# Kernel tuning notes

Measured on AMD Instinct MI355X. Metric: run time of the kernel, lower is better.

## Reference

```python
import jax, jax.numpy as jnp
import numpy as np

D_K = 128
NEG_BIG = 1e32  # matches torch's -1e+32 additive mask (finite in fp32)


def setup_inputs() -> dict:
    key = jax.random.key(0)
    kq, kk, kv, kqp, kkp = jax.random.split(key, 5)
    B, M, N, d_k, d_v = 8, 2048, 2048, D_K, 128
    return {
        "queries": jax.random.normal(kq, (B, M, d_k), dtype=jnp.float32),
        "keys": jax.random.normal(kk, (B, N, d_k), dtype=jnp.float32),
        "values": jax.random.normal(kv, (B, N, d_v), dtype=jnp.float32),
        "q_pres": jax.random.randint(kqp, (B, M), 0, 2, dtype=jnp.int32),
        "k_pres": jax.random.randint(kkp, (B, N), 0, 2, dtype=jnp.int32),
    }


def reference(queries, keys, values, q_pres, k_pres):
    # routing: [B, M, N] = Q K^T with multiplicative presence masking
    routing = jnp.einsum("bmd,bnd->bmn", queries, keys)
    qp = q_pres.astype(jnp.float32)  # [B, M]
    kp = k_pres.astype(jnp.float32)  # [B, N]
    routing = routing * qp[:, :, None]
    routing = routing * kp[:, None, :]
    # additive -1e32 mask for absent keys, then scaled softmax over N
    routing = routing - (1.0 - kp[:, None, :]) * NEG_BIG
    routing = jax.nn.softmax(routing / np.sqrt(D_K).astype(np.float32), axis=-1)
    return jnp.einsum("bmn,bnv->bmv", routing, values)
```

## Files before the change

### kernel.cpp

```cpp
#include <hip/hip_runtime.h>
#include <cstddef>
#include <cstdint>

#define SEQ_M 2048
#define SEQ_N 2048
#define DKV 128
#define BN 64
#define NCH 4
#define CHKEYS (SEQ_N / NCH)
#define NKT 32
#define MT2 16
#define NREC (NCH * 8 * MT2)

typedef _Float16 f16x8 __attribute__((ext_vector_type(8)));
typedef _Float16 f16x4 __attribute__((ext_vector_type(4)));
typedef _Float16 f16x2 __attribute__((ext_vector_type(2)));
typedef float f32x4 __attribute__((ext_vector_type(4)));
typedef float f32x16 __attribute__((ext_vector_type(16)));
typedef unsigned int u32x2 __attribute__((ext_vector_type(2)));
typedef unsigned int u32x4 __attribute__((ext_vector_type(4)));

#if defined(__has_builtin)
#if __has_builtin(__builtin_amdgcn_exp2f)
#define EXP2F(x) __builtin_amdgcn_exp2f(x)
#else
#define EXP2F(x) exp2f(x)
#endif
#else
#define EXP2F(x) exp2f(x)
#endif

#if defined(__has_builtin)
#if __has_builtin(__builtin_amdgcn_permlane32_swap)
#define HAVE_PLSWAP 1
#endif
#endif

#define SM_SCALE 0.12751745f
#define BIG_NEG 1.2751745e31f
#define MSHIFT 8.0f

#define KH_OFF 0
#define VH_OFF (256 * 8192)
#define P16_OFF (2 * 256 * 8192)
#define L_BYTE_OFF ((size_t)(P16_OFF + (size_t)NREC * 16384) * 2)
#define WS_NEED (L_BYTE_OFF + (size_t)NREC * 128 * 4)

#define AS1 __attribute__((address_space(1)))
#define AS3 __attribute__((address_space(3)))

__device__ __forceinline__ void copy16(const void* g, void* lds_base,
                                       void* lds_lane) {
#if defined(__has_builtin) && __has_builtin(__builtin_amdgcn_global_load_lds)
  __builtin_amdgcn_global_load_lds((const AS1 void*)g, (AS3 void*)lds_base, 16,
                                   0, 0);
  (void)lds_lane;
#else
  *(f16x8*)lds_lane = *(const f16x8*)g;
#endif
}

__device__ __forceinline__ void pswap(unsigned int a, unsigned int b, int hi,
                                      unsigned int& o0, unsigned int& o1) {
#if defined(HAVE_PLSWAP)
  u32x2 r = __builtin_amdgcn_permlane32_swap(a, b, false, false);
  o0 = r[0];
  o1 = r[1];
  (void)hi;
#else
  const unsigned int as = __shfl_xor(a, 32);
  const unsigned int bs = __shfl_xor(b, 32);
  o0 = hi ? bs : a;
  o1 = hi ? b : as;
#endif
}

__global__ __launch_bounds__(256) void prep(const float* __restrict__ Kg,
                                            const float* __restrict__ Vg,
                                            _Float16* __restrict__ Kh,
                                            _Float16* __restrict__ Vh) {
  const int T = blockIdx.x >> 2;
  const int kind = blockIdx.x & 1;
  const int half = (blockIdx.x >> 1) & 1;
  const int b = T >> 5, nt = T & 31;
  const int t = threadIdx.x;
  if (kind == 0) {
    const float* Kb = Kg + ((size_t)b * SEQ_N + nt * 64) * DKV;
    _Float16* Kt_ = Kh + (size_t)T * 8192;
#pragma unroll
    for (int i = 0; i < 2; ++i) {
      const int idx = half * 512 + i * 256 + t;
      const int c = idx & 15, key = idx >> 4;
      const float* src = Kb + key * DKV + c * 8;
      const float4 a0 = *(const float4*)src;
      const float4 a1 = *(const float4*)(src + 4);
      f16x8 h;
      h[0] = (_Float16)a0.x; h[1] = (_Float16)a0.y;
      h[2] = (_Float16)a0.z; h[3] = (_Float16)a0.w;
      h[4] = (_Float16)a1.x; h[5] = (_Float16)a1.y;
      h[6] = (_Float16)a1.z; h[7] = (_Float16)a1.w;
      *(f16x8*)&Kt_[c * 512 + key * 8] = h;
    }
  } else {
    const float* Vb = Vg + ((size_t)b * SEQ_N + nt * 64) * DKV;
    _Float16* Vt_ = Vh + (size_t)T * 8192;
#pragma unroll
    for (int i = 0; i < 2; ++i) {
      const int idx = half * 512 + i * 256 + t;
      const int vcol = idx & 127, g = idx >> 7;
      f16x8 h;
#pragma unroll
      for (int j = 0; j < 8; ++j)
        h[j] = (_Float16)Vb[(size_t)(g * 8 + j) * DKV + vcol];
      *(f16x8*)&Vt_[vcol * 64 + ((g ^ (vcol & 7)) * 8)] = h;
    }
  }
}

__global__ __launch_bounds__(256, 2) void attn_core7(
    const _Float16* __restrict__ Kh, const _Float16* __restrict__ Vh,
    const float* __restrict__ Qg, const int* __restrict__ QPg,
    const int* __restrict__ KPg, _Float16* __restrict__ P16,
    float* __restrict__ Lw) {
  __shared__ _Float16 smem[4 * 8192];
  _Float16* const Kt0 = smem;
  _Float16* const Vt0 = smem + 8192;
  _Float16* const Kt1 = smem + 16384;
  _Float16* const Vt1 = smem + 24576;

  const int tid = threadIdx.x;
  const int w = tid >> 6;
  const int lane = tid & 63;
  const int lam = lane & 31;
  const int hi = lane >> 5;

  const int b = blockIdx.x & 7;
  const int rest = blockIdx.x >> 3;
  const int mt = rest & 15;
  const int chk = rest >> 4;

  auto STAGE = [&](int nt, _Float16* ktD, _Float16* vtD) {
    const char* gsrc =
        (w < 2) ? (const char*)(Kh + (size_t)(b * NKT + nt) * 8192) + w * 8192
                : (const char*)(Vh + (size_t)(b * NKT + nt) * 8192) +
                      (w - 2) * 8192;
    char* ldst = (w < 2) ? (char*)ktD + w * 8192 : (char*)vtD + (w - 2) * 8192;
#pragma unroll
    for (int r = 0; r < 8; ++r)
      copy16(gsrc + r * 1024 + lane * 16, ldst + r * 1024,
             ldst + r * 1024 + lane * 16);
  };

  STAGE(chk * 8 + 0, Kt0, Vt0);

  const int qrow = mt * 128 + w * 32 + lam;
  const float* qptr = Qg + ((size_t)b * SEQ_M + qrow) * DKV;
  const float qs = QPg[b * SEQ_M + qrow] ? 1.0f : 0.0f;
  f16x8 qf[8];
#pragma unroll
  for (int ks16 = 0; ks16 < 8; ++ks16) {
    const float* src = qptr + ks16 * 16 + hi * 8;
    const float4 a0 = *(const float4*)src;
    const float4 a1 = *(const float4*)(src + 4);
    f16x8 h;
    h[0] = (_Float16)(a0.x * qs); h[1] = (_Float16)(a0.y * qs);
    h[2] = (_Float16)(a0.z * qs); h[3] = (_Float16)(a0.w * qs);
    h[4] = (_Float16)(a1.x * qs); h[5] = (_Float16)(a1.y * qs);
    h[6] = (_Float16)(a1.z * qs); h[7] = (_Float16)(a1.w * qs);
    qf[ks16] = h;
  }

  unsigned long long km[8];
#pragma unroll
  for (int ti = 0; ti < 8; ++ti)
    km[ti] = __ballot(
        KPg[(size_t)b * SEQ_N + (size_t)(chk * 8 + ti) * 64 + lane] != 0);

  f32x16 o[4];
#pragma unroll
  for (int vt = 0; vt < 4; ++vt)
#pragma unroll
    for (int r = 0; r < 16; ++r) o[vt][r] = 0.f;
  float pl = 0.f;

  __syncthreads();

#pragma unroll
  for (int ti = 0; ti < 8; ++ti) {
    _Float16* const KtC = (ti & 1) ? Kt1 : Kt0;
    _Float16* const VtC = (ti & 1) ? Vt1 : Vt0;
    _Float16* const KtN = (ti & 1) ? Kt0 : Kt1;
    _Float16* const VtN = (ti & 1) ? Vt0 : Vt1;
    if (ti + 1 < 8) STAGE(chk * 8 + ti + 1, KtN, VtN);
    const unsigned long long kmask = km[ti];

    f32x16 st0, st1;
#pragma unroll
    for (int r = 0; r < 16; ++r) { st0[r] = 0.f; st1[r] = 0.f; }
#pragma unroll
    for (int ks16 = 0; ks16 < 8; ++ks16) {
      const f16x8 qv = qf[ks16];
      const int c = ks16 * 2 + hi;
      const f16x8 k0 = *(const f16x8*)&KtC[c * 512 + (0 * 32 + lam) * 8];
      const f16x8 k1 = *(const f16x8*)&KtC[c * 512 + (1 * 32 + lam) * 8];
      st0 = __builtin_amdgcn_mfma_f32_32x32x16_f16(k0, qv, st0, 0, 0, 0);
      st1 = __builtin_amdgcn_mfma_f32_32x32x16_f16(k1, qv, st1, 0, 0, 0);
    }

    float p[2][16];
#pragma unroll
    for (int kt = 0; kt < 2; ++kt)
#pragma unroll
      for (int reg = 0; reg < 16; ++reg) {
        const int keybase = kt * 32 + (reg & 3) + 8 * (reg >> 2);
        const bool b0 = (kmask >> keybase) & 1ull;
        const bool b4 = (kmask >> (keybase + 4)) & 1ull;
        const float s = (kt ? st1[reg] : st0[reg]) * SM_SCALE - MSHIFT;
        const float e = EXP2F(s);
        const float v = (hi ? b4 : b0) ? e : 0.f;
        p[kt][reg] = v;
        pl += v;
      }

    unsigned int pk[2][8];
#pragma unroll
    for (int kt = 0; kt < 2; ++kt)
#pragma unroll
      for (int m = 0; m < 8; ++m) {
        f16x2 hh;
        hh[0] = (_Float16)p[kt][2 * m];
        hh[1] = (_Float16)p[kt][2 * m + 1];
        pk[kt][m] = __builtin_bit_cast(unsigned int, hh);
      }

#pragma unroll
    for (int ks = 0; ks < 4; ++ks) {
      const int kt = ks >> 1, k16 = ks & 1;
      unsigned int f0, f2, f1, f3;
      pswap(pk[kt][4 * k16 + 0], pk[kt][4 * k16 + 2], hi, f0, f2);
      pswap(pk[kt][4 * k16 + 1], pk[kt][4 * k16 + 3], hi, f1, f3);
      const u32x4 pa4 = {f0, f1, f2, f3};
      const f16x8 paf = __builtin_bit_cast(f16x8, pa4);
      const int g = ks * 2 + hi;
#pragma unroll
      for (int vt = 0; vt < 4; ++vt) {
        const int vcol = vt * 32 + lam;
        const f16x8 vf = *(const f16x8*)&VtC[vcol * 64 + ((g ^ (vcol & 7)) * 8)];
        o[vt] = __builtin_amdgcn_mfma_f32_32x32x16_f16(paf, vf, o[vt], 0, 0, 0);
      }
    }
    __syncthreads();
  }

  pl += __shfl_xor(pl, 32);
  const int rec = (chk * 8 + b) * MT2 + mt;
  if (lane < 32) Lw[(size_t)rec * 128 + w * 32 + lam] = pl;
  float li[16];
#pragma unroll
  for (int reg = 0; reg < 16; ++reg)
    li[reg] = 1.0f / __shfl(pl, (reg & 3) + 8 * (reg >> 2) + 4 * hi);

  _Float16* ob = P16 + (size_t)rec * 16384 + (size_t)(w * 32) * 128;
#pragma unroll
  for (int vt = 0; vt < 4; ++vt)
#pragma unroll
    for (int reg = 0; reg < 16; ++reg) {
      const int q = (reg & 3) + 8 * (reg >> 2) + 4 * hi;
      ob[q * 128 + vt * 32 + lam] = (_Float16)(o[vt][reg] * li[reg]);
    }
}

__global__ __launch_bounds__(256) void attn_combine4(
    const _Float16* __restrict__ P16, const float* __restrict__ Lw,
    float* __restrict__ Og) {
  const int t = threadIdx.x;
  const int b = blockIdx.x & 7;
  const int rest = blockIdx.x >> 3;
  const int mt = rest & 15;
  const int ch = rest >> 4;
  __shared__ float lsh[NCH][128];
#pragma unroll
  for (int i = 0; i < 2; ++i) {
    const int idx = i * 256 + t;
    const int c = idx >> 7, row = idx & 127;
    lsh[c][row] = Lw[(size_t)((c * 8 + b) * MT2 + mt) * 128 + row];
  }
  __syncthreads();
  const int colh = ch * 64 + (t & 15) * 4;
  const int rg = t >> 4;
  const _Float16* recO[NCH];
#pragma unroll
  for (int c = 0; c < NCH; ++c)
    recO[c] = P16 + (size_t)((c * 8 + b) * MT2 + mt) * 16384;
  float* outb = Og + ((size_t)b * SEQ_M + mt * 128) * DKV;
#pragma unroll
  for (int rr = 0; rr < 8; ++rr) {
    const int row = rr * 16 + rg;
    float lt = 0.f;
#pragma unroll
    for (int c = 0; c < NCH; ++c) lt += lsh[c][row];
    const float inv = 1.0f / lt;
    f32x4 acc = (f32x4){0.f, 0.f, 0.f, 0.f};
#pragma unroll
    for (int c = 0; c < NCH; ++c) {
      const float wc = lsh[c][row];
      const f16x4 v = *(const f16x4*)(recO[c] + (size_t)row * 128 + colh);
      acc[0] += wc * (float)v[0]; acc[1] += wc * (float)v[1];
      acc[2] += wc * (float)v[2]; acc[3] += wc * (float)v[3];
    }
    f32x4 r;
    r[0] = acc[0] * inv; r[1] = acc[1] * inv;
    r[2] = acc[2] * inv; r[3] = acc[3] * inv;
    *(f32x4*)(outb + (size_t)row * DKV + colh) = r;
  }
}

__global__ __launch_bounds__(256) void attn_fallback(
    const float* __restrict__ Qg, const float* __restrict__ Kg,
    const float* __restrict__ Vg, const int* __restrict__ QPg,
    const int* __restrict__ KPg, float* __restrict__ Og) {
  __shared__ _Float16 smem[16 * 65 * 8 + 128 * 72];
  _Float16* const Kt = smem;
  _Float16* const Vt = smem + 16 * 65 * 8;
  const int tid = threadIdx.x;
  const int w = tid >> 6;
  const int lane = tid & 63;
  const int q16 = lane & 15;
  const int quad = lane >> 4;
  _Float16* const Pl = smem + w * (16 * 72);
  const int b = blockIdx.x & 7;
  const int mb = (blockIdx.x >> 3) * 64;
  const int qrow = mb + w * 16 + q16;
  const float* qptr = Qg + ((size_t)b * SEQ_M + qrow) * DKV;
  const float qs = QPg[b * SEQ_M + qrow] ? 1.0f : 0.0f;
  f16x8 qf[4];
#pragma unroll
  for (int kc = 0; kc < 4; ++kc) {
    const float4 a0 = *(const float4*)(qptr + kc * 32 + quad * 8);
    const float4 a1 = *(const float4*)(qptr + kc * 32 + quad * 8 + 4);
    f16x8 h;
    h[0] = (_Float16)(a0.x * qs); h[1] = (_Float16)(a0.y * qs);
    h[2] = (_Float16)(a0.z * qs); h[3] = (_Float16)(a0.w * qs);
    h[4] = (_Float16)(a1.x * qs); h[5] = (_Float16)(a1.y * qs);
    h[6] = (_Float16)(a1.z * qs); h[7] = (_Float16)(a1.w * qs);
    qf[kc] = h;
  }
  f32x4 o[8];
#pragma unroll
  for (int vt = 0; vt < 8; ++vt) o[vt] = (f32x4){0.f, 0.f, 0.f, 0.f};
  float m_run = -3.0e38f, l_run = 0.f;
  const int kn = tid >> 2, ks = (tid & 3) * 32;
  const int vg = tid >> 3, vk = (tid & 7) * 8;
  for (int n0 = 0; n0 < SEQ_N; n0 += BN) {
    __syncthreads();
    {
      const float* kp_ = Kg + ((size_t)b * SEQ_N + n0 + kn) * DKV + ks;
#pragma unroll
      for (int c2 = 0; c2 < 4; ++c2) {
        const float4 a0 = *(const float4*)(kp_ + c2 * 8);
        const float4 a1 = *(const float4*)(kp_ + c2 * 8 + 4);
        f16x8 h;
        h[0] = (_Float16)a0.x; h[1] = (_Float16)a0.y;
        h[2] = (_Float16)a0.z; h[3] = (_Float16)a0.w;
        h[4] = (_Float16)a1.x; h[5] = (_Float16)a1.y;
        h[6] = (_Float16)a1.z; h[7] = (_Float16)a1.w;
        *(f16x8*)&Kt[(((ks >> 3) + c2) * 65 + kn) * 8] = h;
      }
    }
    {
      const float* vp0 = Vg + ((size_t)b * SEQ_N + n0 + vk) * DKV + vg * 4;
      float4 vv[8];
#pragma unroll
      for (int j = 0; j < 8; ++j) vv[j] = *(const float4*)(vp0 + (size_t)j * DKV);
#pragma unroll
      for (int i = 0; i < 4; ++i) {
        f16x8 h;
#pragma unroll
        for (int j = 0; j < 8; ++j) h[j] = (_Float16)(((const float*)&vv[j])[i]);
        *(f16x8*)&Vt[(vg * 4 + i) * 72 + vk] = h;
      }
    }
    const unsigned long long kmask =
        __ballot(KPg[(size_t)b * SEQ_N + n0 + lane] != 0);
    __syncthreads();
    f32x4 st[4];
#pragma unroll
    for (int t = 0; t < 4; ++t) st[t] = (f32x4){0.f, 0.f, 0.f, 0.f};
#pragma unroll
    for (int kc = 0; kc < 4; ++kc) {
      const f16x8 qv = qf[kc];
#pragma unroll
      for (int t = 0; t < 4; ++t) {
        const f16x8 kf =
            *(const f16x8*)&Kt[((kc * 4 + quad) * 65 + t * 16 + q16) * 8];
        st[t] = __builtin_amdgcn_mfma_f32_16x16x32_f16(kf, qv, st[t], 0, 0, 0);
      }
    }
    float s2[16];
    float mx = -3.0e38f;
#pragma unroll
    for (int t = 0; t < 4; ++t)
#pragma unroll
      for (int r = 0; r < 4; ++r) {
        const int key = t * 16 + quad * 4 + r;
        const float v =
            ((kmask >> key) & 1ull) ? st[t][r] * SM_SCALE : -BIG_NEG;
        s2[t * 4 + r] = v;
        mx = fmaxf(mx, v);
      }
    mx = fmaxf(mx, __shfl_xor(mx, 16));
    mx = fmaxf(mx, __shfl_xor(mx, 32));
    const float mnew = fmaxf(m_run, mx);
    const float alpha = EXP2F(m_run - mnew);
    m_run = mnew;
    float p[16];
    float psum = 0.f;
#pragma unroll
    for (int i = 0; i < 16; ++i) {
      p[i] = EXP2F(s2[i] - mnew);
      psum += p[i];
    }
    psum += __shfl_xor(psum, 16);
    psum += __shfl_xor(psum, 32);
    l_run = l_run * alpha + psum;
    float arow[4];
#pragma unroll
    for (int r = 0; r < 4; ++r) arow[r] = __shfl(alpha, quad * 4 + r);
#pragma unroll
    for (int vt = 0; vt < 8; ++vt) {
      o[vt][0] *= arow[0]; o[vt][1] *= arow[1];
      o[vt][2] *= arow[2]; o[vt][3] *= arow[3];
    }
    __syncthreads();
#pragma unroll
    for (int t = 0; t < 4; ++t) {
      f16x4 pw;
      pw[0] = (_Float16)p[t * 4 + 0];
      pw[1] = (_Float16)p[t * 4 + 1];
      pw[2] = (_Float16)p[t * 4 + 2];
      pw[3] = (_Float16)p[t * 4 + 3];
      *(f16x4*)&Pl[q16 * 72 + t * 16 + quad * 4] = pw;
    }
    const f16x8 pf0 = *(const f16x8*)&Pl[q16 * 72 + quad * 8];
    const f16x8 pf1 = *(const f16x8*)&Pl[q16 * 72 + 32 + quad * 8];
#pragma unroll
    for (int vt = 0; vt < 8; ++vt) {
      const f16x8 v0 = *(const f16x8*)&Vt[(vt * 16 + q16) * 72 + quad * 8];
      o[vt] = __builtin_amdgcn_mfma_f32_16x16x32_f16(pf0, v0, o[vt], 0, 0, 0);
      const f16x8 v1 = *(const f16x8*)&Vt[(vt * 16 + q16) * 72 + 32 + quad * 8];
      o[vt] = __builtin_amdgcn_mfma_f32_16x16x32_f16(pf1, v1, o[vt], 0, 0, 0);
    }
  }
  float linv[4];
#pragma unroll
  for (int r = 0; r < 4; ++r) linv[r] = 1.0f / __shfl(l_run, quad * 4 + r);
  float* obase = Og + ((size_t)b * SEQ_M + mb + w * 16) * DKV;
#pragma unroll
  for (int vt = 0; vt < 8; ++vt)
#pragma unroll
    for (int r = 0; r < 4; ++r)
      obase[(size_t)(quad * 4 + r) * DKV + vt * 16 + q16] = o[vt][r] * linv[r];
}

extern "C" void kernel_launch(void* const* d_in, const int* in_sizes, int n_in,
                              void* d_out, int out_size, void* d_ws,
                              size_t ws_size, hipStream_t stream) {
  const float* Q = (const float*)d_in[0];
  const float* K = (const float*)d_in[1];
  const float* V = (const float*)d_in[2];
  const int* QP = (const int*)d_in[3];
  const int* KP = (const int*)d_in[4];
  float* O = (float*)d_out;
  if (ws_size >= WS_NEED) {
    _Float16* wsh = (_Float16*)d_ws;
    _Float16* Kh = wsh + KH_OFF;
    _Float16* Vh = wsh + VH_OFF;
    _Float16* P16 = wsh + P16_OFF;
    float* Lw = (float*)((char*)d_ws + L_BYTE_OFF);
    prep<<<dim3(1024), dim3(256), 0, stream>>>(K, V, Kh, Vh);
    attn_core7<<<dim3(8 * MT2 * NCH), dim3(256), 0, stream>>>(
        Kh, Vh, Q, QP, KP, P16, Lw);
    attn_combine4<<<dim3(8 * MT2 * 2), dim3(256), 0, stream>>>(P16, Lw, O);
  } else {
    attn_fallback<<<dim3(8 * 32), dim3(256), 0, stream>>>(Q, K, V, QP, KP, O);
  }
}
```

Before: 111.1 us.

## Split attention block across 8 waves with column-split PV output

The core kernel now launches 512 threads: pairs of waves share the same 32 query rows and each computes half of the 128 value columns, so per-wave output accumulators drop from four to two tiles. Each wave pair redundantly recomputes QK^T scores and the exp for its rows, and the K/V staging is spread over eight waves. The exp/mask/pack loop is also fused so probabilities are converted to fp16 directly without a temporary array. The aim is more resident waves per CU to hide latency, at the cost of duplicated QK^T MFMA and softmax work.

```diff
diff --git a/kernel.cpp b/kernel.cpp
--- a/kernel.cpp
+++ b/kernel.cpp
@@ -117,7 +117,7 @@
   }
 }
 
-__global__ __launch_bounds__(256, 2) void attn_core7(
+__global__ __launch_bounds__(512, 4) void attn_core8(
     const _Float16* __restrict__ Kh, const _Float16* __restrict__ Vh,
     const float* __restrict__ Qg, const int* __restrict__ QPg,
     const int* __restrict__ KPg, _Float16* __restrict__ P16,
@@ -130,6 +130,8 @@
 
   const int tid = threadIdx.x;
   const int w = tid >> 6;
+  const int rg = w >> 1;
+  const int cg = w & 1;
   const int lane = tid & 63;
   const int lam = lane & 31;
   const int hi = lane >> 5;
@@ -141,19 +143,21 @@
 
   auto STAGE = [&](int nt, _Float16* ktD, _Float16* vtD) {
     const char* gsrc =
-        (w < 2) ? (const char*)(Kh + (size_t)(b * NKT + nt) * 8192) + w * 8192
+        (w < 4) ? (const char*)(Kh + (size_t)(b * NKT + nt) * 8192) +
+                      (w & 3) * 4096
                 : (const char*)(Vh + (size_t)(b * NKT + nt) * 8192) +
-                      (w - 2) * 8192;
-    char* ldst = (w < 2) ? (char*)ktD + w * 8192 : (char*)vtD + (w - 2) * 8192;
-#pragma unroll
-    for (int r = 0; r < 8; ++r)
+                      (w & 3) * 4096;
+    char* ldst = (w < 4) ? (char*)ktD + (w & 3) * 4096
+                         : (char*)vtD + (w & 3) * 4096;
+#pragma unroll
+    for (int r = 0; r < 4; ++r)
       copy16(gsrc + r * 1024 + lane * 16, ldst + r * 1024,
              ldst + r * 1024 + lane * 16);
   };
 
   STAGE(chk * 8 + 0, Kt0, Vt0);
 
-  const int qrow = mt * 128 + w * 32 + lam;
+  const int qrow = mt * 128 + rg * 32 + lam;
   const float* qptr = Qg + ((size_t)b * SEQ_M + qrow) * DKV;
   const float qs = QPg[b * SEQ_M + qrow] ? 1.0f : 0.0f;
   f16x8 qf[8];
@@ -176,9 +180,9 @@
     km[ti] = __ballot(
         KPg[(size_t)b * SEQ_N + (size_t)(chk * 8 + ti) * 64 + lane] != 0);
 
-  f32x16 o[4];
-#pragma unroll
-  for (int vt = 0; vt < 4; ++vt)
+  f32x16 o[2];
+#pragma unroll
+  for (int vt = 0; vt < 2; ++vt)
 #pragma unroll
     for (int r = 0; r < 16; ++r) o[vt][r] = 0.f;
   float pl = 0.f;
@@ -207,29 +211,22 @@
       st1 = __builtin_amdgcn_mfma_f32_32x32x16_f16(k1, qv, st1, 0, 0, 0);
     }
 
-    float p[2][16];
+    unsigned int pk[2][8];
 #pragma unroll
     for (int kt = 0; kt < 2; ++kt)
 #pragma unroll
-      for (int reg = 0; reg < 16; ++reg) {
-        const int keybase = kt * 32 + (reg & 3) + 8 * (reg >> 2);
-        const bool b0 = (kmask >> keybase) & 1ull;
-        const bool b4 = (kmask >> (keybase + 4)) & 1ull;
-        const float s = (kt ? st1[reg] : st0[reg]) * SM_SCALE - MSHIFT;
-        const float e = EXP2F(s);
-        const float v = (hi ? b4 : b0) ? e : 0.f;
-        p[kt][reg] = v;
-        pl += v;
-      }
-
-    unsigned int pk[2][8];
-#pragma unroll
-    for (int kt = 0; kt < 2; ++kt)
-#pragma unroll
       for (int m = 0; m < 8; ++m) {
+        const int r0 = 2 * m, r1 = 2 * m + 1;
+        const int key0 = kt * 32 + (r0 & 3) + 8 * (r0 >> 2) + 4 * hi;
+        const int key1 = kt * 32 + (r1 & 3) + 8 * (r1 >> 2) + 4 * hi;
+        const float s0 = (kt ? st1[r0] : st0[r0]) * SM_SCALE - MSHIFT;
+        const float s1 = (kt ? st1[r1] : st0[r1]) * SM_SCALE - MSHIFT;
+        const float e0 = ((kmask >> key0) & 1ull) ? EXP2F(s0) : 0.f;
+        const float e1 = ((kmask >> key1) & 1ull) ? EXP2F(s1) : 0.f;
+        pl += e0 + e1;
         f16x2 hh;
-        hh[0] = (_Float16)p[kt][2 * m];
-        hh[1] = (_Float16)p[kt][2 * m + 1];
+        hh[0] = (_Float16)e0;
+        hh[1] = (_Float16)e1;
         pk[kt][m] = __builtin_bit_cast(unsigned int, hh);
       }
 
@@ -243,8 +240,8 @@
       const f16x8 paf = __builtin_bit_cast(f16x8, pa4);
       const int g = ks * 2 + hi;
 #pragma unroll
-      for (int vt = 0; vt < 4; ++vt) {
-        const int vcol = vt * 32 + lam;
+      for (int vt = 0; vt < 2; ++vt) {
+        const int vcol = cg * 64 + vt * 32 + lam;
         const f16x8 vf = *(const f16x8*)&VtC[vcol * 64 + ((g ^ (vcol & 7)) * 8)];
         o[vt] = __builtin_amdgcn_mfma_f32_32x32x16_f16(paf, vf, o[vt], 0, 0, 0);
       }
@@ -254,19 +251,19 @@
 
   pl += __shfl_xor(pl, 32);
   const int rec = (chk * 8 + b) * MT2 + mt;
-  if (lane < 32) Lw[(size_t)rec * 128 + w * 32 + lam] = pl;
+  if (cg == 0 && lane < 32) Lw[(size_t)rec * 128 + rg * 32 + lam] = pl;
   float li[16];
 #pragma unroll
   for (int reg = 0; reg < 16; ++reg)
     li[reg] = 1.0f / __shfl(pl, (reg & 3) + 8 * (reg >> 2) + 4 * hi);
 
-  _Float16* ob = P16 + (size_t)rec * 16384 + (size_t)(w * 32) * 128;
-#pragma unroll
-  for (int vt = 0; vt < 4; ++vt)
+  _Float16* ob = P16 + (size_t)rec * 16384 + (size_t)(rg * 32) * 128;
+#pragma unroll
+  for (int vt = 0; vt < 2; ++vt)
 #pragma unroll
     for (int reg = 0; reg < 16; ++reg) {
       const int q = (reg & 3) + 8 * (reg >> 2) + 4 * hi;
-      ob[q * 128 + vt * 32 + lam] = (_Float16)(o[vt][reg] * li[reg]);
+      ob[q * 128 + cg * 64 + vt * 32 + lam] = (_Float16)(o[vt][reg] * li[reg]);
     }
 }
 
@@ -478,7 +475,7 @@
     _Float16* P16 = wsh + P16_OFF;
     float* Lw = (float*)((char*)d_ws + L_BYTE_OFF);
     prep<<<dim3(1024), dim3(256), 0, stream>>>(K, V, Kh, Vh);
-    attn_core7<<<dim3(8 * MT2 * NCH), dim3(256), 0, stream>>>(
+    attn_core8<<<dim3(8 * MT2 * NCH), dim3(512), 0, stream>>>(
         Kh, Vh, Q, QP, KP, P16, Lw);
     attn_combine4<<<dim3(8 * MT2 * 2), dim3(256), 0, stream>>>(P16, Lw, O);
   } else {
```

Result: slower. 182.9 us (+64.7%).

## Roll key-tile loop, load key masks per tile, raise wave priority around MFMA

Applied to the files above, without the earlier changes.

The main attention loop is no longer fully unrolled. LDS buffer pointers are swapped at the end of each iteration instead of being picked by parity. The eight precomputed ballot key masks are replaced by a ballot inside each iteration, and exp/mask/pack are fused into one pass. s_setprio is raised around the two MFMA phases to favour matrix issue over the softmax work of other waves. Together these cut register pressure and code size, at the cost of a global load plus ballot in every iteration and some loss of cross-iteration scheduling.

```diff
diff --git a/kernel.cpp b/kernel.cpp
--- a/kernel.cpp
+++ b/kernel.cpp
@@ -59,6 +59,16 @@
   *(f16x8*)lds_lane = *(const f16x8*)g;
 #endif
 }
+
+#if defined(__has_builtin)
+#if __has_builtin(__builtin_amdgcn_s_setprio)
+#define SETPRIO(x) __builtin_amdgcn_s_setprio(x)
+#else
+#define SETPRIO(x)
+#endif
+#else
+#define SETPRIO(x)
+#endif
 
 __device__ __forceinline__ void pswap(unsigned int a, unsigned int b, int hi,
                                       unsigned int& o0, unsigned int& o1) {
@@ -117,7 +127,7 @@
   }
 }
 
-__global__ __launch_bounds__(256, 2) void attn_core7(
+__global__ __launch_bounds__(256, 2) void attn_core11(
     const _Float16* __restrict__ Kh, const _Float16* __restrict__ Vh,
     const float* __restrict__ Qg, const int* __restrict__ QPg,
     const int* __restrict__ KPg, _Float16* __restrict__ P16,
@@ -170,12 +180,6 @@
     qf[ks16] = h;
   }
 
-  unsigned long long km[8];
-#pragma unroll
-  for (int ti = 0; ti < 8; ++ti)
-    km[ti] = __ballot(
-        KPg[(size_t)b * SEQ_N + (size_t)(chk * 8 + ti) * 64 + lane] != 0);
-
   f32x16 o[4];
 #pragma unroll
   for (int vt = 0; vt < 4; ++vt)
@@ -185,18 +189,19 @@
 
   __syncthreads();
 
-#pragma unroll
+  _Float16* KtC = Kt0;
+  _Float16* VtC = Vt0;
+  _Float16* KtN = Kt1;
+  _Float16* VtN = Vt1;
   for (int ti = 0; ti < 8; ++ti) {
-    _Float16* const KtC = (ti & 1) ? Kt1 : Kt0;
-    _Float16* const VtC = (ti & 1) ? Vt1 : Vt0;
-    _Float16* const KtN = (ti & 1) ? Kt0 : Kt1;
-    _Float16* const VtN = (ti & 1) ? Vt0 : Vt1;
     if (ti + 1 < 8) STAGE(chk * 8 + ti + 1, KtN, VtN);
-    const unsigned long long kmask = km[ti];
+    const unsigned long long kmask = __ballot(
+        KPg[(size_t)b * SEQ_N + (size_t)(chk * 8 + ti) * 64 + lane] != 0);
 
     f32x16 st0, st1;
 #pragma unroll
     for (int r = 0; r < 16; ++r) { st0[r] = 0.f; st1[r] = 0.f; }
+    SETPRIO(1);
 #pragma unroll
     for (int ks16 = 0; ks16 < 8; ++ks16) {
       const f16x8 qv = qf[ks16];
@@ -206,33 +211,28 @@
       st0 = __builtin_amdgcn_mfma_f32_32x32x16_f16(k0, qv, st0, 0, 0, 0);
       st1 = __builtin_amdgcn_mfma_f32_32x32x16_f16(k1, qv, st1, 0, 0, 0);
     }
-
-    float p[2][16];
+    SETPRIO(0);
+
+    unsigned int pk[2][8];
 #pragma unroll
     for (int kt = 0; kt < 2; ++kt)
 #pragma unroll
-      for (int reg = 0; reg < 16; ++reg) {
-        const int keybase = kt * 32 + (reg & 3) + 8 * (reg >> 2);
-        const bool b0 = (kmask >> keybase) & 1ull;
-        const bool b4 = (kmask >> (keybase + 4)) & 1ull;
-        const float s = (kt ? st1[reg] : st0[reg]) * SM_SCALE - MSHIFT;
-        const float e = EXP2F(s);
-        const float v = (hi ? b4 : b0) ? e : 0.f;
-        p[kt][reg] = v;
-        pl += v;
-      }
-
-    unsigned int pk[2][8];
-#pragma unroll
-    for (int kt = 0; kt < 2; ++kt)
-#pragma unroll
       for (int m = 0; m < 8; ++m) {
+        const int r0 = 2 * m, r1 = 2 * m + 1;
+        const int key0 = kt * 32 + (r0 & 3) + 8 * (r0 >> 2) + 4 * hi;
+        const int key1 = kt * 32 + (r1 & 3) + 8 * (r1 >> 2) + 4 * hi;
+        const float s0 = (kt ? st1[r0] : st0[r0]) * SM_SCALE - MSHIFT;
+        const float s1 = (kt ? st1[r1] : st0[r1]) * SM_SCALE - MSHIFT;
+        const float e0 = ((kmask >> key0) & 1ull) ? EXP2F(s0) : 0.f;
+        const float e1 = ((kmask >> key1) & 1ull) ? EXP2F(s1) : 0.f;
+        pl += e0 + e1;
         f16x2 hh;
-        hh[0] = (_Float16)p[kt][2 * m];
-        hh[1] = (_Float16)p[kt][2 * m + 1];
+        hh[0] = (_Float16)e0;
+        hh[1] = (_Float16)e1;
         pk[kt][m] = __builtin_bit_cast(unsigned int, hh);
       }
 
+    SETPRIO(1);
 #pragma unroll
     for (int ks = 0; ks < 4; ++ks) {
       const int kt = ks >> 1, k16 = ks & 1;
@@ -249,7 +249,10 @@
         o[vt] = __builtin_amdgcn_mfma_f32_32x32x16_f16(paf, vf, o[vt], 0, 0, 0);
       }
     }
+    SETPRIO(0);
     __syncthreads();
+    _Float16* tk = KtC; KtC = KtN; KtN = tk;
+    _Float16* tv = VtC; VtC = VtN; VtN = tv;
   }
 
   pl += __shfl_xor(pl, 32);
@@ -478,7 +481,7 @@
     _Float16* P16 = wsh + P16_OFF;
     float* Lw = (float*)((char*)d_ws + L_BYTE_OFF);
     prep<<<dim3(1024), dim3(256), 0, stream>>>(K, V, Kh, Vh);
-    attn_core7<<<dim3(8 * MT2 * NCH), dim3(256), 0, stream>>>(
+    attn_core11<<<dim3(8 * MT2 * NCH), dim3(256), 0, stream>>>(
         Kh, Vh, Q, QP, KP, P16, Lw);
     attn_combine4<<<dim3(8 * MT2 * 2), dim3(256), 0, stream>>>(P16, Lw, O);
   } else {
```

Measured after the change: 110.1 us. Within noise of the previous version (-0.8%).
